# Performance work log

Measured on AMD Instinct MI355X. Metric: run time of the kernel, lower is better.

The kernel has to match this reference:

```python
import jax, jax.numpy as jnp
import numpy as np

B, R, S, L, H, A, TD = 4, 8, 8, 256, 768, 256, 100


def setup_inputs() -> dict:
    key = jax.random.key(0)
    ks = iter(jax.random.split(key, 64))
    n = lambda *s: jax.random.normal(next(ks), s, jnp.float32)
    p = lambda *s: jax.random.normal(next(ks), s, jnp.float32) * 0.02
    inp = {
        'X': n(B, L, H),
        'X_mean': n(B, H),
        'mask': jnp.ones((B, L), jnp.float32),
        'sk': jax.random.randint(next(ks), (B, R, S, 2), 0, L, dtype=jnp.int32),
        'sk_mask': jnp.ones((B, R, S), jnp.float32),
        'semantic_rel_emb': n(R, H),
        'transe_rel_emb': n(R, TD),
    }
    # 4 EntityExtractors (reconstructed as two H->1 linears producing start/end logits)
    for pref in ('fh', 'bt', 'ft', 'bh'):
        inp[pref + '_ws'] = p(H); inp[pref + '_bs'] = p()
        inp[pref + '_we'] = p(H); inp[pref + '_be'] = p()
    # 2 RelationAttentions (fwd: rel_dim=H, bwd: rel_dim=TD)
    for pref, rd in (('fra', H), ('bra', TD)):
        inp[pref + '_Wx'] = p(H, A);  inp[pref + '_bx'] = p(A)
        inp[pref + '_Wr'] = p(rd, A); inp[pref + '_br'] = p(A)
        inp[pref + '_Wg'] = p(H, A);  inp[pref + '_bg'] = p(A)
        inp[pref + '_V'] = p(A);      inp[pref + '_bv'] = p()
    # 2 FuseExtractors
    for pref in ('ffe', 'bfe'):
        inp[pref + '_Ws'] = p(H, H); inp[pref + '_bs'] = p(H)
        inp[pref + '_Wx'] = p(H, H); inp[pref + '_bx'] = p(H)
    return inp


def _entity(h, ws, bs, we, be):
    # EntityExtractor: start/end logits over last (H) axis
    return jnp.einsum('...h,h->...', h, ws) + bs, jnp.einsum('...h,h->...', h, we) + be


def _rel_attn(X, rel, g, Wx, bx, Wr, br, Wg, bg, V, bv):
    wx = X @ Wx + bx          # (B,L,A)
    wr = rel @ Wr + br        # (R,A)
    wg = g @ Wg + bg          # (B,A)
    z = jnp.tanh(wx[:, None, :, :] + wr[None, :, None, :] + wg[:, None, None, :])  # (B,R,L,A)
    e = jnp.einsum('brla,a->brl', z, V) + bv
    a = jax.nn.softmax(e, axis=-1)                       # (B,R,L)
    c = jnp.einsum('brl,blh->brh', a, X)                 # (B,R,H)
    return c, a


def _sk_to_embeddings(sk, sk_mask, X):
    # vectorized span-endpoint gather + average (replaces B*R*S python loop)
    b_idx = jnp.arange(X.shape[0])[:, None, None]        # (B,1,1)
    emb = (X[b_idx, sk[..., 0]] + X[b_idx, sk[..., 1]]) * 0.5   # (B,R,S,H)
    return sk_mask[..., None] * emb


def _fuse(X, c, sk_embs, sk_mask, Ws, bs, Wx, bx):
    w_x = X @ Wx + bx                                    # (B,L,H)
    w_sk = (sk_embs @ Ws + bs) * sk_mask[..., None]      # (B,R,S,H)
    # h_ijk = Ws*sk + Wx*x_i + c_j + x_i  -> (B,R,S,L,H)
    return (w_sk[:, :, :, None, :] + w_x[:, None, None, :, :]
            + c[:, :, None, None, :] + X[:, None, None, :, :])


def reference(X, X_mean, mask, sk, sk_mask, semantic_rel_emb, transe_rel_emb,
              fh_ws, fh_bs, fh_we, fh_be, bt_ws, bt_bs, bt_we, bt_be,
              ft_ws, ft_bs, ft_we, ft_be, bh_ws, bh_bs, bh_we, bh_be,
              fra_Wx, fra_bx, fra_Wr, fra_br, fra_Wg, fra_bg, fra_V, fra_bv,
              bra_Wx, bra_bx, bra_Wr, bra_br, bra_Wg, bra_bg, bra_V, bra_bv,
              ffe_Ws, ffe_bs, ffe_Wx, ffe_bx, bfe_Ws, bfe_bs, bfe_Wx, bfe_bx):
    fh_s, fh_e = _entity(X, fh_ws, fh_bs, fh_we, fh_be)      # (B,L)
    bt_s, bt_e = _entity(X, bt_ws, bt_bs, bt_we, bt_be)      # (B,L)
    fwd_c, _ = _rel_attn(X, semantic_rel_emb, X_mean,
                         fra_Wx, fra_bx, fra_Wr, fra_br, fra_Wg, fra_bg, fra_V, fra_bv)
    bwd_c, _ = _rel_attn(X, transe_rel_emb, X_mean,
                         bra_Wx, bra_bx, bra_Wr, bra_br, bra_Wg, bra_bg, bra_V, bra_bv)
    sk_embs = _sk_to_embeddings(sk, sk_mask, X)              # (B,R,S,H)
    fwd_hijk = _fuse(X, fwd_c, sk_embs, sk_mask, ffe_Ws, ffe_bs, ffe_Wx, ffe_bx)
    bwd_hijk = _fuse(X, bwd_c, sk_embs, sk_mask, bfe_Ws, bfe_bs, bfe_Wx, bfe_bx)
    ft_s, ft_e = _entity(fwd_hijk, ft_ws, ft_bs, ft_we, ft_be)  # (B,R,S,L)
    bh_s, bh_e = _entity(bwd_hijk, bh_ws, bh_bs, bh_we, bh_be)  # (B,R,S,L)
    return (fh_s, fh_e, bt_s, bt_e, ft_s, ft_e, bh_s, bh_e)
```

## Files before the change

kernel.cpp:

```cpp
#include <hip/hip_runtime.h>
#include <hip/hip_bf16.h>

#define NB 4
#define NR 8
#define NS 8
#define NL 256
#define NH 768
#define NA 256
#define NTD 100

#define WX_F 0
#define WX_B (WX_F + NB*NL*NA)
#define WR_F (WX_B + NB*NL*NA)
#define WR_B (WR_F + NR*NA)
#define WG_F (WR_B + NR*NA)
#define WG_B (WG_F + NB*NA)
#define C_F  (WG_B + NB*NA)
#define C_B  (C_F + NB*NR*NH)
#define QV   (C_B + NB*NR*NH)
#define SCAL (QV + 8*NH)
#define DXL  (SCAL + 8)
#define ATT16 (DXL + 4*NB*NL)
#define XB   (ATT16 + 16384)
#define WT   (XB + (NB*NL*NH)/2)
#define XT   (WT + (2*NA*NH)/2)

#define O_FT_S 4096
#define O_FT_E 69632
#define O_BH_S 135168
#define O_BH_E 200704

typedef __attribute__((ext_vector_type(8))) short short8;
typedef __attribute__((ext_vector_type(4))) float f32x4;

struct bh4 { __hip_bfloat16 a, b, c, d; };

__device__ __forceinline__ float tanh_fast(float x) {
    x = fminf(15.f, fmaxf(-15.f, x));
    float t = __expf(2.f * x);
    return (t - 1.f) / (t + 1.f);
}

__device__ __forceinline__ float wave_reduce(float v) {
    #pragma unroll
    for (int off = 32; off > 0; off >>= 1) v += __shfl_down(v, off);
    return v;
}

__global__ void __launch_bounds__(512) k_setup(const float* __restrict__ X,
                      const float* __restrict__ fra_Wx, const float* __restrict__ bra_Wx,
                      const float* __restrict__ sem, const float* __restrict__ transe,
                      const float* __restrict__ X_mean,
                      const float* __restrict__ fra_Wr, const float* __restrict__ fra_br,
                      const float* __restrict__ fra_Wg, const float* __restrict__ fra_bg,
                      const float* __restrict__ bra_Wr, const float* __restrict__ bra_br,
                      const float* __restrict__ bra_Wg, const float* __restrict__ bra_bg,
                      const float* __restrict__ ffe_Ws, const float* __restrict__ ffe_bs,
                      const float* __restrict__ ffe_Wx, const float* __restrict__ ffe_bx,
                      const float* __restrict__ bfe_Ws, const float* __restrict__ bfe_bs,
                      const float* __restrict__ bfe_Wx, const float* __restrict__ bfe_bx,
                      const float* __restrict__ ft_ws, const float* __restrict__ ft_we,
                      const float* __restrict__ bh_ws, const float* __restrict__ bh_we,
                      float* __restrict__ ws) {
    __shared__ float smem[2112];
    const int bid = blockIdx.x, tid = threadIdx.x;

    if (bid < 384) {
        __hip_bfloat16* xb = (__hip_bfloat16*)(ws + XB);
        const int i0 = bid*2048 + tid*4;
        const float4 v = *(const float4*)(X + i0);
        bh4 o = { __float2bfloat16(v.x), __float2bfloat16(v.y),
                  __float2bfloat16(v.z), __float2bfloat16(v.w) };
        *(bh4*)(xb + i0) = o;
    } else if (bid < 576) {
        __hip_bfloat16* wt = (__hip_bfloat16*)(ws + WT);
        const int t2 = bid - 384;
        const int mt = t2 / 96;
        const int half = tid >> 8, tid2 = tid & 255;
        const int tile = (t2 % 96)*2 + half;
        const int h0 = (tile >> 3) * 32, c0 = (tile & 7) * 32;
        const float* W = mt ? bra_Wx : fra_Wx;
        float (*sh)[33] = (float(*)[33])(smem + half*1056);
        const int r = tid2 >> 5, c = tid2 & 31;
        #pragma unroll
        for (int i = 0; i < 4; ++i)
            sh[r + 8*i][c] = W[(size_t)(h0 + r + 8*i)*NA + c0 + c];
        __syncthreads();
        #pragma unroll
        for (int i = 0; i < 4; ++i)
            wt[(size_t)(mt*NA + c0 + r + 8*i)*NH + h0 + c] = __float2bfloat16(sh[c][r + 8*i]);
    } else if (bid < 960) {
        __hip_bfloat16* xt = (__hip_bfloat16*)(ws + XT);
        const int t2 = bid - 576;
        const int half = tid >> 8, tid2 = tid & 255;
        const int tile = t2*2 + half;
        const int b = tile / 192, trem = tile % 192;
        const int h0 = (trem >> 3) * 32, l0 = (trem & 7) * 32;
        float (*sh)[33] = (float(*)[33])(smem + half*1056);
        const int r = tid2 >> 5, c = tid2 & 31;
        #pragma unroll
        for (int i = 0; i < 4; ++i)
            sh[r + 8*i][c] = X[(size_t)(b*NL + l0 + r + 8*i)*NH + h0 + c];
        __syncthreads();
        #pragma unroll
        for (int i = 0; i < 4; ++i)
            xt[(size_t)(b*NH + h0 + r + 8*i)*NL + l0 + c] = __float2bfloat16(sh[c][r + 8*i]);
    } else if (bid < 984) {
        float* sh = smem;
        float* red2 = smem + 768;
        const int q = bid - 960;
        const float* s; const float* W; const float* bias; float* out; int K;
        if (q < 8)       { s = sem + q*NH;         W = fra_Wr; bias = fra_br; out = ws + WR_F + q*NA;      K = NH;  }
        else if (q < 16) { s = transe + (q-8)*NTD; W = bra_Wr; bias = bra_br; out = ws + WR_B + (q-8)*NA;  K = NTD; }
        else if (q < 20) { s = X_mean + (q-16)*NH; W = fra_Wg; bias = fra_bg; out = ws + WG_F + (q-16)*NA; K = NH;  }
        else             { s = X_mean + (q-20)*NH; W = bra_Wg; bias = bra_bg; out = ws + WG_B + (q-20)*NA; K = NH;  }
        for (int j = tid; j < K; j += 512) sh[j] = s[j];
        __syncthreads();
        const int half = tid >> 8, col = tid & 255;
        const int khalf = (K/2) & ~15;
        const int k0 = half ? khalf : 0, k1 = half ? K : khalf;
        const float* Wc = W + col;
        float acc = 0.f;
        int k = k0;
        for (; k + 16 <= k1; k += 16) {
            float wb[16];
            #pragma unroll
            for (int i = 0; i < 16; ++i) wb[i] = Wc[(size_t)(k+i)*NA];
            #pragma unroll
            for (int i = 0; i < 16; ++i) acc += sh[k+i] * wb[i];
        }
        for (; k < k1; ++k) acc += sh[k] * Wc[(size_t)k*NA];
        red2[half*256 + col] = acc;
        __syncthreads();
        if (half == 0) out[col] = red2[col] + red2[256 + col] + bias[col];
    } else if (bid < 992) {
        float* red2 = smem;
        const int q = bid - 984;
        const float* a; const float* b2;
        switch (q) {
            case 0: a = ffe_bs; b2 = ft_ws; break;
            case 1: a = ffe_bs; b2 = ft_we; break;
            case 2: a = ffe_bx; b2 = ft_ws; break;
            case 3: a = ffe_bx; b2 = ft_we; break;
            case 4: a = bfe_bs; b2 = bh_ws; break;
            case 5: a = bfe_bs; b2 = bh_we; break;
            case 6: a = bfe_bx; b2 = bh_ws; break;
            default: a = bfe_bx; b2 = bh_we; break;
        }
        float p = a[tid]*b2[tid];
        if (tid < 256) p += a[tid+512]*b2[tid+512];
        red2[tid] = p; __syncthreads();
        for (int s2 = 256; s2 > 0; s2 >>= 1) { if (tid < s2) red2[tid] += red2[tid + s2]; __syncthreads(); }
        if (tid == 0) ws[SCAL + q] = red2[0];
    } else {
        const int idx = bid - 992;
        const int mi = idx / 96;
        const int row = (idx % 96)*8 + (tid >> 6);
        const int lane = tid & 63;
        const float* M; const float* v0; const float* v1; bool self;
        switch (mi) {
            case 0: M = ffe_Ws; v0 = ft_ws; v1 = ft_we; self = false; break;
            case 1: M = bfe_Ws; v0 = bh_ws; v1 = bh_we; self = false; break;
            case 2: M = ffe_Wx; v0 = ft_ws; v1 = ft_we; self = true;  break;
            default: M = bfe_Wx; v0 = bh_ws; v1 = bh_we; self = true; break;
        }
        const float4* mr4 = (const float4*)(M + (size_t)row*NH);
        const float4* va4 = (const float4*)v0;
        const float4* vb4 = (const float4*)v1;
        float a0 = 0.f, a1 = 0.f;
        #pragma unroll
        for (int i = 0; i < 3; ++i) {
            const float4 m4 = mr4[lane + 64*i];
            const float4 x4 = va4[lane + 64*i];
            const float4 y4 = vb4[lane + 64*i];
            a0 += m4.x*x4.x + m4.y*x4.y + m4.z*x4.z + m4.w*x4.w;
            a1 += m4.x*y4.x + m4.y*y4.y + m4.z*y4.z + m4.w*y4.w;
        }
        a0 = wave_reduce(a0); a1 = wave_reduce(a1);
        if (lane == 0) {
            ws[QV + (mi*2 + 0)*NH + row] = a0 + (self ? v0[row] : 0.f);
            ws[QV + (mi*2 + 1)*NH + row] = a1 + (self ? v1[row] : 0.f);
        }
    }
}

__global__ void __launch_bounds__(256) k_wx(const float* __restrict__ fra_bx,
                                            const float* __restrict__ bra_bx,
                                            float* __restrict__ ws) {
    const __hip_bfloat16* xb = (const __hip_bfloat16*)(ws + XB);
    const __hip_bfloat16* wt = (const __hip_bfloat16*)(ws + WT);
    const int bid = blockIdx.x, tid = threadIdx.x;
    const int fb = bid >> 8;
    const int rt = (bid & 255) >> 2, cg = bid & 3;
    const int wv = tid >> 6, lane = tid & 63;
    const int m0 = rt * 16, c0 = cg * 64 + wv * 16;
    const int r16 = lane & 15, koff = (lane >> 4) * 8;

    const short8* ap = (const short8*)(xb + (size_t)(m0 + r16)*NH + koff);
    const short8* bp = (const short8*)(wt + (size_t)(fb*NA + c0 + r16)*NH + koff);

    f32x4 acc = {0.f, 0.f, 0.f, 0.f};
    #pragma unroll
    for (int ks = 0; ks < 24; ks += 4) {
        short8 a0 = ap[(ks+0)*4], b0 = bp[(ks+0)*4];
        short8 a1 = ap[(ks+1)*4], b1 = bp[(ks+1)*4];
        short8 a2 = ap[(ks+2)*4], b2 = bp[(ks+2)*4];
        short8 a3 = ap[(ks+3)*4], b3 = bp[(ks+3)*4];
        acc = __builtin_amdgcn_mfma_f32_16x16x32_bf16(a0, b0, acc, 0, 0, 0);
        acc = __builtin_amdgcn_mfma_f32_16x16x32_bf16(a1, b1, acc, 0, 0, 0);
        acc = __builtin_amdgcn_mfma_f32_16x16x32_bf16(a2, b2, acc, 0, 0, 0);
        acc = __builtin_amdgcn_mfma_f32_16x16x32_bf16(a3, b3, acc, 0, 0, 0);
    }
    const float* bia = fb ? bra_bx : fra_bx;
    float* outp = ws + (fb ? WX_B : WX_F);
    const int col = c0 + r16;
    const float bb = bia[col];
    const int rbase = m0 + (lane >> 4) * 4;
    #pragma unroll
    for (int j = 0; j < 4; ++j)
        outp[(size_t)(rbase + j)*NA + col] = acc[j] + bb;
}

__global__ void __launch_bounds__(512) k_attn(const float* __restrict__ fra_V, const float* __restrict__ fra_bv,
                       const float* __restrict__ bra_V, const float* __restrict__ bra_bv,
                       float* __restrict__ ws) {
    __shared__ float wa_s[NA], v_s[NA], red[NL], part[NL];
    const int bid = blockIdx.x, tid = threadIdx.x;
    const int fb = bid >> 5, b = (bid >> 3) & 3, r = bid & 7;
    const int l = tid & 255, half = tid >> 8;

    const float* wr = ws + (fb ? WR_B : WR_F) + r*NA;
    const float* wg = ws + (fb ? WG_B : WG_F) + b*NA;
    const float* V  = fb ? bra_V : fra_V;
    const float  bv = fb ? bra_bv[0] : fra_bv[0];
    const float* wxp = ws + (fb ? WX_B : WX_F);

    if (tid < 256) { wa_s[tid] = wr[tid] + wg[tid]; v_s[tid] = V[tid]; }
    __syncthreads();

    const float4* wxrow = (const float4*)(wxp + (size_t)(b*NL + l)*NA + half*128);
    float acc = 0.f;
    for (int a0 = 0; a0 < 32; a0 += 8) {
        float4 wb[8];
        #pragma unroll
        for (int i = 0; i < 8; ++i) wb[i] = wxrow[a0 + i];
        #pragma unroll
        for (int i = 0; i < 8; ++i) {
            const int a = half*128 + (a0 + i)*4;
            acc += tanh_fast(wb[i].x + wa_s[a+0]) * v_s[a+0];
            acc += tanh_fast(wb[i].y + wa_s[a+1]) * v_s[a+1];
            acc += tanh_fast(wb[i].z + wa_s[a+2]) * v_s[a+2];
            acc += tanh_fast(wb[i].w + wa_s[a+3]) * v_s[a+3];
        }
    }
    if (half) part[l] = acc;
    __syncthreads();

    float e = 0.f;
    if (!half) e = acc + part[l] + bv;
    if (tid < 256) red[tid] = e;
    __syncthreads();
    for (int s2 = 128; s2 > 0; s2 >>= 1) { if (tid < s2) red[tid] = fmaxf(red[tid], red[tid+s2]); __syncthreads(); }
    const float mx = red[0];
    __syncthreads();
    float p = 0.f;
    if (tid < 256) { p = __expf(e - mx); red[tid] = p; }
    __syncthreads();
    for (int s2 = 128; s2 > 0; s2 >>= 1) { if (tid < s2) red[tid] += red[tid+s2]; __syncthreads(); }
    if (tid < 256) {
        __hip_bfloat16* att = (__hip_bfloat16*)(ws + ATT16);
        const int g = fb*NB + b;
        att[(size_t)(g*16 + r)*NL + tid]     = __float2bfloat16(p / red[0]);
        att[(size_t)(g*16 + 8 + r)*NL + tid] = __float2bfloat16(0.f);
    }
}

__global__ void __launch_bounds__(256) k_ctx(float* __restrict__ ws) {
    const __hip_bfloat16* att = (const __hip_bfloat16*)(ws + ATT16);
    const __hip_bfloat16* xt  = (const __hip_bfloat16*)(ws + XT);
    const int bid = blockIdx.x, tid = threadIdx.x;
    const int g = bid / 12, hc = bid % 12;
    const int fb = g >> 2, b = g & 3;
    const int wv = tid >> 6, lane = tid & 63;
    const int h0 = hc*64 + wv*16;
    const int r16 = lane & 15, khi = lane >> 4;

    const short8* ap = (const short8*)(att + (size_t)(g*16 + r16)*NL) + khi;
    const short8* bp = (const short8*)(xt + (size_t)(b*NH + h0 + r16)*NL) + khi;

    f32x4 acc = {0.f, 0.f, 0.f, 0.f};
    #pragma unroll
    for (int ks = 0; ks < 8; ++ks) {
        short8 af = ap[ks*4];
        short8 bf = bp[ks*4];
        acc = __builtin_amdgcn_mfma_f32_16x16x32_bf16(af, bf, acc, 0, 0, 0);
    }
    float* cc = ws + (fb ? C_B : C_F) + (size_t)b*NR*NH;
    const int col = h0 + r16;
    const int rbase = khi * 4;
    #pragma unroll
    for (int j = 0; j < 4; ++j) {
        const int r = rbase + j;
        if (r < 8) cc[(size_t)r*NH + col] = acc[j];
    }
}

__global__ void __launch_bounds__(256) k_dxl(const float* __restrict__ X,
                      const float* __restrict__ fh_ws, const float* __restrict__ fh_bs,
                      const float* __restrict__ fh_we, const float* __restrict__ fh_be,
                      const float* __restrict__ bt_ws, const float* __restrict__ bt_bs,
                      const float* __restrict__ bt_we, const float* __restrict__ bt_be,
                      float* __restrict__ ws, float* __restrict__ out) {
    __shared__ float xr[NH];
    const int m = blockIdx.x;
    const int tid = threadIdx.x, w = tid >> 6, lane = tid & 63;

    if (tid < 192) ((float4*)xr)[tid] = ((const float4*)(X + (size_t)m*NH))[tid];
    __syncthreads();

    const float* v0; const float* v1; float add0, add1; float* o0; float* o1;
    if (w == 0)      { v0 = fh_ws; add0 = fh_bs[0]; o0 = out;        v1 = fh_we; add1 = fh_be[0]; o1 = out + 1024; }
    else if (w == 1) { v0 = bt_ws; add0 = bt_bs[0]; o0 = out + 2048; v1 = bt_we; add1 = bt_be[0]; o1 = out + 3072; }
    else if (w == 2) { v0 = ws + QV + 4*NH; add0 = ws[SCAL+2]; o0 = ws + DXL;
                       v1 = ws + QV + 5*NH; add1 = ws[SCAL+3]; o1 = ws + DXL + 1024; }
    else             { v0 = ws + QV + 6*NH; add0 = ws[SCAL+6]; o0 = ws + DXL + 2048;
                       v1 = ws + QV + 7*NH; add1 = ws[SCAL+7]; o1 = ws + DXL + 3072; }

    const float4* xr4 = (const float4*)xr;
    const float4* v04 = (const float4*)v0;
    const float4* v14 = (const float4*)v1;
    float a0 = 0.f, a1 = 0.f;
    #pragma unroll
    for (int i = 0; i < 3; ++i) {
        const float4 x4 = xr4[lane + 64*i];
        const float4 p4 = v04[lane + 64*i];
        const float4 q4 = v14[lane + 64*i];
        a0 += x4.x*p4.x + x4.y*p4.y + x4.z*p4.z + x4.w*p4.w;
        a1 += x4.x*q4.x + x4.y*q4.y + x4.z*q4.z + x4.w*q4.w;
    }
    a0 = wave_reduce(a0); a1 = wave_reduce(a1);
    if (lane == 0) { o0[m] = a0 + add0; o1[m] = a1 + add1; }
}

__global__ void __launch_bounds__(256) k_skf(const float* __restrict__ X, const int* __restrict__ sk,
                     const float* __restrict__ sk_mask,
                     const float* __restrict__ ft_ws, const float* __restrict__ ft_bs,
                     const float* __restrict__ ft_we, const float* __restrict__ ft_be,
                     const float* __restrict__ bh_ws, const float* __restrict__ bh_bs,
                     const float* __restrict__ bh_we, const float* __restrict__ bh_be,
                     const float* __restrict__ ws, float* __restrict__ out) {
    __shared__ float avg[NH];
    __shared__ float d1_s[4], d3_s[4];
    const int brs = blockIdx.x;
    const int tid = threadIdx.x, w = tid >> 6, lane = tid & 63;
    const int b = brs >> 6, br = brs >> 3;
    const int i0 = sk[brs*2], i1 = sk[brs*2 + 1];
    const float mk = sk_mask[brs];

    if (tid < 192) {
        const float4 x0 = ((const float4*)(X + (size_t)(b*NL + i0)*NH))[tid];
        const float4 x1 = ((const float4*)(X + (size_t)(b*NL + i1)*NH))[tid];
        float4 o; o.x = 0.5f*(x0.x+x1.x); o.y = 0.5f*(x0.y+x1.y);
        o.z = 0.5f*(x0.z+x1.z); o.w = 0.5f*(x0.w+x1.w);
        ((float4*)avg)[tid] = o;
    }
    __syncthreads();

    const float4* q4 = (const float4*)(ws + QV + w*NH);
    const float4* av4 = (const float4*)avg;
    const float4* c4 = (const float4*)(ws + ((w < 2) ? C_F : C_B) + (size_t)br*NH);
    const float* v = (w == 0) ? ft_ws : (w == 1) ? ft_we : (w == 2) ? bh_ws : bh_we;
    const float4* vv4 = (const float4*)v;
    float acc = 0.f, d = 0.f;
    #pragma unroll
    for (int i = 0; i < 3; ++i) {
        const float4 a4 = av4[lane + 64*i];
        const float4 b4 = q4[lane + 64*i];
        const float4 e4 = c4[lane + 64*i];
        const float4 f4 = vv4[lane + 64*i];
        acc += a4.x*b4.x + a4.y*b4.y + a4.z*b4.z + a4.w*b4.w;
        d   += e4.x*f4.x + e4.y*f4.y + e4.z*f4.z + e4.w*f4.w;
    }
    acc = wave_reduce(acc); d = wave_reduce(d);
    if (lane == 0) {
        const float bsdot = ws[SCAL + ((w < 2) ? w : (w + 2))];
        d1_s[w] = mk*mk*acc + mk*bsdot;
        d3_s[w] = d;
    }
    __syncthreads();

    const int l = tid, m = b*NL + l, o = brs*NL + l;
    out[O_FT_S + o] = d1_s[0] + ws[DXL + 0*1024 + m] + d3_s[0] + ft_bs[0];
    out[O_FT_E + o] = d1_s[1] + ws[DXL + 1*1024 + m] + d3_s[1] + ft_be[0];
    out[O_BH_S + o] = d1_s[2] + ws[DXL + 2*1024 + m] + d3_s[2] + bh_bs[0];
    out[O_BH_E + o] = d1_s[3] + ws[DXL + 3*1024 + m] + d3_s[3] + bh_be[0];
}

extern "C" void kernel_launch(void* const* d_in, const int* in_sizes, int n_in,
                              void* d_out, int out_size, void* d_ws, size_t ws_size,
                              hipStream_t stream) {
    const float* X        = (const float*)d_in[0];
    const float* X_mean   = (const float*)d_in[1];
    const int*   sk       = (const int*)d_in[3];
    const float* sk_mask  = (const float*)d_in[4];
    const float* sem      = (const float*)d_in[5];
    const float* transe   = (const float*)d_in[6];
    const float* fh_ws = (const float*)d_in[7],  *fh_bs = (const float*)d_in[8];
    const float* fh_we = (const float*)d_in[9],  *fh_be = (const float*)d_in[10];
    const float* bt_ws = (const float*)d_in[11], *bt_bs = (const float*)d_in[12];
    const float* bt_we = (const float*)d_in[13], *bt_be = (const float*)d_in[14];
    const float* ft_ws = (const float*)d_in[15], *ft_bs = (const float*)d_in[16];
    const float* ft_we = (const float*)d_in[17], *ft_be = (const float*)d_in[18];
    const float* bh_ws = (const float*)d_in[19], *bh_bs = (const float*)d_in[20];
    const float* bh_we = (const float*)d_in[21], *bh_be = (const float*)d_in[22];
    const float* fra_Wx = (const float*)d_in[23], *fra_bx = (const float*)d_in[24];
    const float* fra_Wr = (const float*)d_in[25], *fra_br = (const float*)d_in[26];
    const float* fra_Wg = (const float*)d_in[27], *fra_bg = (const float*)d_in[28];
    const float* fra_V  = (const float*)d_in[29], *fra_bv = (const float*)d_in[30];
    const float* bra_Wx = (const float*)d_in[31], *bra_bx = (const float*)d_in[32];
    const float* bra_Wr = (const float*)d_in[33], *bra_br = (const float*)d_in[34];
    const float* bra_Wg = (const float*)d_in[35], *bra_bg = (const float*)d_in[36];
    const float* bra_V  = (const float*)d_in[37], *bra_bv = (const float*)d_in[38];
    const float* ffe_Ws = (const float*)d_in[39], *ffe_bs = (const float*)d_in[40];
    const float* ffe_Wx = (const float*)d_in[41], *ffe_bx = (const float*)d_in[42];
    const float* bfe_Ws = (const float*)d_in[43], *bfe_bs = (const float*)d_in[44];
    const float* bfe_Wx = (const float*)d_in[45], *bfe_bx = (const float*)d_in[46];

    float* out = (float*)d_out;
    float* ws  = (float*)d_ws;

    k_setup<<<dim3(1376), dim3(512), 0, stream>>>(X, fra_Wx, bra_Wx, sem, transe, X_mean,
        fra_Wr, fra_br, fra_Wg, fra_bg, bra_Wr, bra_br, bra_Wg, bra_bg,
        ffe_Ws, ffe_bs, ffe_Wx, ffe_bx, bfe_Ws, bfe_bs, bfe_Wx, bfe_bx,
        ft_ws, ft_we, bh_ws, bh_we, ws);

    k_wx<<<dim3(512), dim3(256), 0, stream>>>(fra_bx, bra_bx, ws);

    k_attn<<<dim3(64), dim3(512), 0, stream>>>(fra_V, fra_bv, bra_V, bra_bv, ws);

    k_ctx<<<dim3(96), dim3(256), 0, stream>>>(ws);

    k_dxl<<<dim3(1024), dim3(256), 0, stream>>>(X, fh_ws, fh_bs, fh_we, fh_be,
        bt_ws, bt_bs, bt_we, bt_be, ws, out);

    k_skf<<<dim3(256), dim3(256), 0, stream>>>(X, sk, sk_mask,
        ft_ws, ft_bs, ft_we, ft_be, bh_ws, bh_bs, bh_we, bh_be, ws, out);
}
```

Before: 205.1 us.

## Fuse X bf16 cast into transpose blocks and merge dxl into wx kernel

The separate block range that cast X to bf16 is removed; the X-transpose blocks now write the row-major bf16 copy while loading tiles, so X is read once instead of twice and the setup grid shrinks. The per-row dot-product kernel (k_dxl) is merged into the MFMA projection kernel as extra blocks, removing one kernel launch and letting the two independent workloads share the GPU. The bf16 row-major writes from the transpose blocks are 2-byte scattered stores, which are less coalesced than the old vectorized cast.

```diff
diff --git a/kernel.cpp b/kernel.cpp
--- a/kernel.cpp
+++ b/kernel.cpp
@@ -32,8 +32,6 @@
 
 typedef __attribute__((ext_vector_type(8))) short short8;
 typedef __attribute__((ext_vector_type(4))) float f32x4;
-
-struct bh4 { __hip_bfloat16 a, b, c, d; };
 
 __device__ __forceinline__ float tanh_fast(float x) {
     x = fminf(15.f, fmaxf(-15.f, x));
@@ -65,19 +63,11 @@
     __shared__ float smem[2112];
     const int bid = blockIdx.x, tid = threadIdx.x;
 
-    if (bid < 384) {
-        __hip_bfloat16* xb = (__hip_bfloat16*)(ws + XB);
-        const int i0 = bid*2048 + tid*4;
-        const float4 v = *(const float4*)(X + i0);
-        bh4 o = { __float2bfloat16(v.x), __float2bfloat16(v.y),
-                  __float2bfloat16(v.z), __float2bfloat16(v.w) };
-        *(bh4*)(xb + i0) = o;
-    } else if (bid < 576) {
+    if (bid < 192) {
         __hip_bfloat16* wt = (__hip_bfloat16*)(ws + WT);
-        const int t2 = bid - 384;
-        const int mt = t2 / 96;
+        const int mt = bid / 96;
         const int half = tid >> 8, tid2 = tid & 255;
-        const int tile = (t2 % 96)*2 + half;
+        const int tile = (bid % 96)*2 + half;
         const int h0 = (tile >> 3) * 32, c0 = (tile & 7) * 32;
         const float* W = mt ? bra_Wx : fra_Wx;
         float (*sh)[33] = (float(*)[33])(smem + half*1056);
@@ -89,9 +79,10 @@
         #pragma unroll
         for (int i = 0; i < 4; ++i)
             wt[(size_t)(mt*NA + c0 + r + 8*i)*NH + h0 + c] = __float2bfloat16(sh[c][r + 8*i]);
-    } else if (bid < 960) {
+    } else if (bid < 576) {
+        __hip_bfloat16* xb = (__hip_bfloat16*)(ws + XB);
         __hip_bfloat16* xt = (__hip_bfloat16*)(ws + XT);
-        const int t2 = bid - 576;
+        const int t2 = bid - 192;
         const int half = tid >> 8, tid2 = tid & 255;
         const int tile = t2*2 + half;
         const int b = tile / 192, trem = tile % 192;
@@ -99,16 +90,19 @@
         float (*sh)[33] = (float(*)[33])(smem + half*1056);
         const int r = tid2 >> 5, c = tid2 & 31;
         #pragma unroll
-        for (int i = 0; i < 4; ++i)
-            sh[r + 8*i][c] = X[(size_t)(b*NL + l0 + r + 8*i)*NH + h0 + c];
+        for (int i = 0; i < 4; ++i) {
+            const float v = X[(size_t)(b*NL + l0 + r + 8*i)*NH + h0 + c];
+            sh[r + 8*i][c] = v;
+            xb[(size_t)(b*NL + l0 + r + 8*i)*NH + h0 + c] = __float2bfloat16(v);
+        }
         __syncthreads();
         #pragma unroll
         for (int i = 0; i < 4; ++i)
             xt[(size_t)(b*NH + h0 + r + 8*i)*NL + l0 + c] = __float2bfloat16(sh[c][r + 8*i]);
-    } else if (bid < 984) {
+    } else if (bid < 600) {
         float* sh = smem;
         float* red2 = smem + 768;
-        const int q = bid - 960;
+        const int q = bid - 576;
         const float* s; const float* W; const float* bias; float* out; int K;
         if (q < 8)       { s = sem + q*NH;         W = fra_Wr; bias = fra_br; out = ws + WR_F + q*NA;      K = NH;  }
         else if (q < 16) { s = transe + (q-8)*NTD; W = bra_Wr; bias = bra_br; out = ws + WR_B + (q-8)*NA;  K = NTD; }
@@ -133,9 +127,9 @@
         red2[half*256 + col] = acc;
         __syncthreads();
         if (half == 0) out[col] = red2[col] + red2[256 + col] + bias[col];
-    } else if (bid < 992) {
+    } else if (bid < 608) {
         float* red2 = smem;
-        const int q = bid - 984;
+        const int q = bid - 600;
         const float* a; const float* b2;
         switch (q) {
             case 0: a = ffe_bs; b2 = ft_ws; break;
@@ -153,7 +147,7 @@
         for (int s2 = 256; s2 > 0; s2 >>= 1) { if (tid < s2) red2[tid] += red2[tid + s2]; __syncthreads(); }
         if (tid == 0) ws[SCAL + q] = red2[0];
     } else {
-        const int idx = bid - 992;
+        const int idx = bid - 608;
         const int mi = idx / 96;
         const int row = (idx % 96)*8 + (tid >> 6);
         const int lane = tid & 63;
@@ -184,41 +178,80 @@
     }
 }
 
-__global__ void __launch_bounds__(256) k_wx(const float* __restrict__ fra_bx,
-                                            const float* __restrict__ bra_bx,
-                                            float* __restrict__ ws) {
-    const __hip_bfloat16* xb = (const __hip_bfloat16*)(ws + XB);
-    const __hip_bfloat16* wt = (const __hip_bfloat16*)(ws + WT);
-    const int bid = blockIdx.x, tid = threadIdx.x;
-    const int fb = bid >> 8;
-    const int rt = (bid & 255) >> 2, cg = bid & 3;
-    const int wv = tid >> 6, lane = tid & 63;
-    const int m0 = rt * 16, c0 = cg * 64 + wv * 16;
-    const int r16 = lane & 15, koff = (lane >> 4) * 8;
-
-    const short8* ap = (const short8*)(xb + (size_t)(m0 + r16)*NH + koff);
-    const short8* bp = (const short8*)(wt + (size_t)(fb*NA + c0 + r16)*NH + koff);
-
-    f32x4 acc = {0.f, 0.f, 0.f, 0.f};
-    #pragma unroll
-    for (int ks = 0; ks < 24; ks += 4) {
-        short8 a0 = ap[(ks+0)*4], b0 = bp[(ks+0)*4];
-        short8 a1 = ap[(ks+1)*4], b1 = bp[(ks+1)*4];
-        short8 a2 = ap[(ks+2)*4], b2 = bp[(ks+2)*4];
-        short8 a3 = ap[(ks+3)*4], b3 = bp[(ks+3)*4];
-        acc = __builtin_amdgcn_mfma_f32_16x16x32_bf16(a0, b0, acc, 0, 0, 0);
-        acc = __builtin_amdgcn_mfma_f32_16x16x32_bf16(a1, b1, acc, 0, 0, 0);
-        acc = __builtin_amdgcn_mfma_f32_16x16x32_bf16(a2, b2, acc, 0, 0, 0);
-        acc = __builtin_amdgcn_mfma_f32_16x16x32_bf16(a3, b3, acc, 0, 0, 0);
-    }
-    const float* bia = fb ? bra_bx : fra_bx;
-    float* outp = ws + (fb ? WX_B : WX_F);
-    const int col = c0 + r16;
-    const float bb = bia[col];
-    const int rbase = m0 + (lane >> 4) * 4;
-    #pragma unroll
-    for (int j = 0; j < 4; ++j)
-        outp[(size_t)(rbase + j)*NA + col] = acc[j] + bb;
+__global__ void __launch_bounds__(256) k_wx_dxl(const float* __restrict__ fra_bx,
+                      const float* __restrict__ bra_bx,
+                      const float* __restrict__ X,
+                      const float* __restrict__ fh_ws, const float* __restrict__ fh_bs,
+                      const float* __restrict__ fh_we, const float* __restrict__ fh_be,
+                      const float* __restrict__ bt_ws, const float* __restrict__ bt_bs,
+                      const float* __restrict__ bt_we, const float* __restrict__ bt_be,
+                      float* __restrict__ ws, float* __restrict__ out) {
+    __shared__ float xr[NH];
+    const int tid = threadIdx.x;
+
+    if (blockIdx.x < 512) {
+        const __hip_bfloat16* xb = (const __hip_bfloat16*)(ws + XB);
+        const __hip_bfloat16* wt = (const __hip_bfloat16*)(ws + WT);
+        const int bid = blockIdx.x;
+        const int fb = bid >> 8;
+        const int rt = (bid & 255) >> 2, cg = bid & 3;
+        const int wv = tid >> 6, lane = tid & 63;
+        const int m0 = rt * 16, c0 = cg * 64 + wv * 16;
+        const int r16 = lane & 15, koff = (lane >> 4) * 8;
+
+        const short8* ap = (const short8*)(xb + (size_t)(m0 + r16)*NH + koff);
+        const short8* bp = (const short8*)(wt + (size_t)(fb*NA + c0 + r16)*NH + koff);
+
+        f32x4 acc = {0.f, 0.f, 0.f, 0.f};
+        #pragma unroll
+        for (int ks = 0; ks < 24; ks += 4) {
+            short8 a0 = ap[(ks+0)*4], b0 = bp[(ks+0)*4];
+            short8 a1 = ap[(ks+1)*4], b1 = bp[(ks+1)*4];
+            short8 a2 = ap[(ks+2)*4], b2 = bp[(ks+2)*4];
+            short8 a3 = ap[(ks+3)*4], b3 = bp[(ks+3)*4];
+            acc = __builtin_amdgcn_mfma_f32_16x16x32_bf16(a0, b0, acc, 0, 0, 0);
+            acc = __builtin_amdgcn_mfma_f32_16x16x32_bf16(a1, b1, acc, 0, 0, 0);
+            acc = __builtin_amdgcn_mfma_f32_16x16x32_bf16(a2, b2, acc, 0, 0, 0);
+            acc = __builtin_amdgcn_mfma_f32_16x16x32_bf16(a3, b3, acc, 0, 0, 0);
+        }
+        const float* bia = fb ? bra_bx : fra_bx;
+        float* outp = ws + (fb ? WX_B : WX_F);
+        const int col = c0 + r16;
+        const float bb = bia[col];
+        const int rbase = m0 + (lane >> 4) * 4;
+        #pragma unroll
+        for (int j = 0; j < 4; ++j)
+            outp[(size_t)(rbase + j)*NA + col] = acc[j] + bb;
+    } else {
+        const int m = blockIdx.x - 512;
+        const int w = tid >> 6, lane = tid & 63;
+
+        if (tid < 192) ((float4*)xr)[tid] = ((const float4*)(X + (size_t)m*NH))[tid];
+        __syncthreads();
+
+        const float* v0; const float* v1; float add0, add1; float* o0; float* o1;
+        if (w == 0)      { v0 = fh_ws; add0 = fh_bs[0]; o0 = out;        v1 = fh_we; add1 = fh_be[0]; o1 = out + 1024; }
+        else if (w == 1) { v0 = bt_ws; add0 = bt_bs[0]; o0 = out + 2048; v1 = bt_we; add1 = bt_be[0]; o1 = out + 3072; }
+        else if (w == 2) { v0 = ws + QV + 4*NH; add0 = ws[SCAL+2]; o0 = ws + DXL;
+                           v1 = ws + QV + 5*NH; add1 = ws[SCAL+3]; o1 = ws + DXL + 1024; }
+        else             { v0 = ws + QV + 6*NH; add0 = ws[SCAL+6]; o0 = ws + DXL + 2048;
+                           v1 = ws + QV + 7*NH; add1 = ws[SCAL+7]; o1 = ws + DXL + 3072; }
+
+        const float4* xr4 = (const float4*)xr;
+        const float4* v04 = (const float4*)v0;
+        const float4* v14 = (const float4*)v1;
+        float a0 = 0.f, a1 = 0.f;
+        #pragma unroll
+        for (int i = 0; i < 3; ++i) {
+            const float4 x4 = xr4[lane + 64*i];
+            const float4 p4 = v04[lane + 64*i];
+            const float4 q4 = v14[lane + 64*i];
+            a0 += x4.x*p4.x + x4.y*p4.y + x4.z*p4.z + x4.w*p4.w;
+            a1 += x4.x*q4.x + x4.y*q4.y + x4.z*q4.z + x4.w*q4.w;
+        }
+        a0 = wave_reduce(a0); a1 = wave_reduce(a1);
+        if (lane == 0) { o0[m] = a0 + add0; o1[m] = a1 + add1; }
+    }
 }
 
 __global__ void __launch_bounds__(512) k_attn(const float* __restrict__ fra_V, const float* __restrict__ fra_bv,
@@ -303,43 +336,6 @@
         const int r = rbase + j;
         if (r < 8) cc[(size_t)r*NH + col] = acc[j];
     }
-}
-
-__global__ void __launch_bounds__(256) k_dxl(const float* __restrict__ X,
-                      const float* __restrict__ fh_ws, const float* __restrict__ fh_bs,
-                      const float* __restrict__ fh_we, const float* __restrict__ fh_be,
-                      const float* __restrict__ bt_ws, const float* __restrict__ bt_bs,
-                      const float* __restrict__ bt_we, const float* __restrict__ bt_be,
-                      float* __restrict__ ws, float* __restrict__ out) {
-    __shared__ float xr[NH];
-    const int m = blockIdx.x;
-    const int tid = threadIdx.x, w = tid >> 6, lane = tid & 63;
-
-    if (tid < 192) ((float4*)xr)[tid] = ((const float4*)(X + (size_t)m*NH))[tid];
-    __syncthreads();
-
-    const float* v0; const float* v1; float add0, add1; float* o0; float* o1;
-    if (w == 0)      { v0 = fh_ws; add0 = fh_bs[0]; o0 = out;        v1 = fh_we; add1 = fh_be[0]; o1 = out + 1024; }
-    else if (w == 1) { v0 = bt_ws; add0 = bt_bs[0]; o0 = out + 2048; v1 = bt_we; add1 = bt_be[0]; o1 = out + 3072; }
-    else if (w == 2) { v0 = ws + QV + 4*NH; add0 = ws[SCAL+2]; o0 = ws + DXL;
-                       v1 = ws + QV + 5*NH; add1 = ws[SCAL+3]; o1 = ws + DXL + 1024; }
-    else             { v0 = ws + QV + 6*NH; add0 = ws[SCAL+6]; o0 = ws + DXL + 2048;
-                       v1 = ws + QV + 7*NH; add1 = ws[SCAL+7]; o1 = ws + DXL + 3072; }
-
-    const float4* xr4 = (const float4*)xr;
-    const float4* v04 = (const float4*)v0;
-    const float4* v14 = (const float4*)v1;
-    float a0 = 0.f, a1 = 0.f;
-    #pragma unroll
-    for (int i = 0; i < 3; ++i) {
-        const float4 x4 = xr4[lane + 64*i];
-        const float4 p4 = v04[lane + 64*i];
-        const float4 q4 = v14[lane + 64*i];
-        a0 += x4.x*p4.x + x4.y*p4.y + x4.z*p4.z + x4.w*p4.w;
-        a1 += x4.x*q4.x + x4.y*q4.y + x4.z*q4.z + x4.w*q4.w;
-    }
-    a0 = wave_reduce(a0); a1 = wave_reduce(a1);
-    if (lane == 0) { o0[m] = a0 + add0; o1[m] = a1 + add1; }
 }
 
 __global__ void __launch_bounds__(256) k_skf(const float* __restrict__ X, const int* __restrict__ sk,
@@ -429,19 +425,17 @@
     float* out = (float*)d_out;
     float* ws  = (float*)d_ws;
 
-    k_setup<<<dim3(1376), dim3(512), 0, stream>>>(X, fra_Wx, bra_Wx, sem, transe, X_mean,
+    k_setup<<<dim3(992), dim3(512), 0, stream>>>(X, fra_Wx, bra_Wx, sem, transe, X_mean,
         fra_Wr, fra_br, fra_Wg, fra_bg, bra_Wr, bra_br, bra_Wg, bra_bg,
         ffe_Ws, ffe_bs, ffe_Wx, ffe_bx, bfe_Ws, bfe_bs, bfe_Wx, bfe_bx,
         ft_ws, ft_we, bh_ws, bh_we, ws);
 
-    k_wx<<<dim3(512), dim3(256), 0, stream>>>(fra_bx, bra_bx, ws);
+    k_wx_dxl<<<dim3(1536), dim3(256), 0, stream>>>(fra_bx, bra_bx, X,
+        fh_ws, fh_bs, fh_we, fh_be, bt_ws, bt_bs, bt_we, bt_be, ws, out);
 
     k_attn<<<dim3(64), dim3(512), 0, stream>>>(fra_V, fra_bv, bra_V, bra_bv, ws);
 
     k_ctx<<<dim3(96), dim3(256), 0, stream>>>(ws);
-
-    k_dxl<<<dim3(1024), dim3(256), 0, stream>>>(X, fh_ws, fh_bs, fh_we, fh_be,
-        bt_ws, bt_bs, bt_we, bt_be, ws, out);
 
     k_skf<<<dim3(256), dim3(256), 0, stream>>>(X, sk, sk_mask,
         ft_ws, ft_bs, ft_we, ft_be, bh_ws, bh_bs, bh_we, bh_be, ws, out);
```

Result: no change. 203.0 us (-1.0%).
